# Performance work log

Hardware: AMD Instinct MI355X
Metric: run time of the kernel (lower is better)

Reference implementation:

```python
import jax, jax.numpy as jnp
import numpy as np

N, C, H, W = 4, 128, 64, 64
HEADS, KS, RED = 4, 7, 18
D = C // HEADS


def _layernorm(x, w, b, eps=1e-5):
    mu = x.mean(axis=-1, keepdims=True)
    var = ((x - mu) ** 2).mean(axis=-1, keepdims=True)
    return (x - mu) * jax.lax.rsqrt(var + eps) * w + b


def _gelu(x):
    return jax.nn.gelu(x, approximate=False)


def setup_inputs() -> dict:
    key = jax.random.key(0)
    ks = jax.random.split(key, 16)
    s = 0.02
    inp = {
        'x': jax.random.normal(ks[0], (N, C, H, W), jnp.float32),
        'ln1_w': jnp.ones((C,), jnp.float32), 'ln1_b': jnp.zeros((C,), jnp.float32),
        'ln2_w': jnp.ones((C,), jnp.float32), 'ln2_b': jnp.zeros((C,), jnp.float32),
        'qkv_w': jax.random.normal(ks[1], (C, 3 * C), jnp.float32) * s,
        'qkv_b': jnp.zeros((3 * C,), jnp.float32),
        'proj_w': jax.random.normal(ks[2], (C, C), jnp.float32) * s,
        'proj_b': jnp.zeros((C,), jnp.float32),
        'rpb': jax.random.normal(ks[3], (HEADS, 2 * KS - 1, 2 * KS - 1), jnp.float32) * s,
        'conv1_w': jax.random.normal(ks[4], (C, C // 4), jnp.float32) * s,
        'conv1_b': jnp.zeros((C // 4,), jnp.float32),
        'conv2_w': jax.random.normal(ks[5], (C // 4, C), jnp.float32) * s,
        'conv2_b': jnp.zeros((C,), jnp.float32),
        'ca1_w': jax.random.normal(ks[6], (C, C // RED), jnp.float32) * s,
        'ca1_b': jnp.zeros((C // RED,), jnp.float32),
        'ca2_w': jax.random.normal(ks[7], (C // RED, C), jnp.float32) * s,
        'ca2_b': jnp.zeros((C,), jnp.float32),
        'fc1_w': jax.random.normal(ks[8], (C, 4 * C), jnp.float32) * s,
        'fc1_b': jnp.zeros((4 * C,), jnp.float32),
        'fc2_w': jax.random.normal(ks[9], (4 * C, C), jnp.float32) * s,
        'fc2_b': jnp.zeros((C,), jnp.float32),
    }
    return inp


def _na2d(xc, qkv_w, qkv_b, rpb, proj_w, proj_b):
    # xc: [N, H, W, C] -> neighborhood attention with clamped k x k windows (NATTEN semantics)
    n, h, w, c = xc.shape
    qkv = (xc @ qkv_w + qkv_b).reshape(n, h, w, 3, HEADS, D)
    q, k, v = qkv[..., 0, :, :], qkv[..., 1, :, :], qkv[..., 2, :, :]
    q = q * (D ** -0.5)
    half = KS // 2
    ni = jnp.clip(jnp.arange(h) - half, 0, h - KS)          # window start per query row
    nj = jnp.clip(jnp.arange(w) - half, 0, w - KS)
    idx_i = ni[:, None] + jnp.arange(KS)                     # [H, KS]
    idx_j = nj[:, None] + jnp.arange(KS)                     # [W, KS]
    # gather key/value windows: [N, H, KS, W, KS, heads, D]
    kw = k[:, idx_i][:, :, :, idx_j]
    vw = v[:, idx_i][:, :, :, idx_j]
    attn = jnp.einsum('nijhd,niajbhd->nijhab', q, kw)        # [N,H,W,heads,KS,KS]
    bi = idx_i - jnp.arange(h)[:, None] + (KS - 1)           # rel-pos bias row index [H,KS]
    bj = idx_j - jnp.arange(w)[:, None] + (KS - 1)           # [W,KS]
    bias = rpb[:, bi][:, :, :, bj]                           # [heads,H,KS,W,KS]
    attn = attn + bias.transpose(1, 3, 0, 2, 4)[None]        # -> [1,H,W,heads,KS,KS]
    attn = jax.nn.softmax(attn.reshape(n, h, w, HEADS, KS * KS), axis=-1)
    attn = attn.reshape(n, h, w, HEADS, KS, KS)
    out = jnp.einsum('nijhab,niajbhd->nijhd', attn, vw).reshape(n, h, w, c)
    return out @ proj_w + proj_b


def reference(x, ln1_w, ln1_b, ln2_w, ln2_b, qkv_w, qkv_b, proj_w, proj_b, rpb,
              conv1_w, conv1_b, conv2_w, conv2_b, ca1_w, ca1_b, ca2_w, ca2_b,
              fc1_w, fc1_b, fc2_w, fc2_b):
    n, c, h, w = x.shape
    xs = x.transpose(0, 2, 3, 1).reshape(n, h * w, c)        # n (h w) c
    shortcut = xs
    xn = _layernorm(xs, ln1_w, ln1_b)
    xc = xn.reshape(n, h, w, c)
    # conv branch: 1x1 -> GELU -> 1x1 -> channel attention
    t = _gelu(xc @ conv1_w + conv1_b) @ conv2_w + conv2_b
    g = t.mean(axis=(1, 2))                                  # global avg pool [N,C]
    g = jax.nn.sigmoid(jax.nn.relu(g @ ca1_w + ca1_b) @ ca2_w + ca2_b)
    ca_x = (t * g[:, None, None, :]).reshape(n, h * w, c)
    # neighborhood attention branch
    na_x = _na2d(xc, qkv_w, qkv_b, rpb, proj_w, proj_b).reshape(n, h * w, c)
    x2 = shortcut + na_x + ca_x * 0.02
    m = _gelu(_layernorm(x2, ln2_w, ln2_b) @ fc1_w + fc1_b) @ fc2_w + fc2_b
    x3 = x2 + m
    return x3.reshape(n, h, w, c).transpose(0, 3, 1, 2)
```

## Files before the change

kernel.cpp:

```cpp
#include <hip/hip_runtime.h>
#include <hip/hip_bf16.h>
#include <math.h>

#define NB 4
#define CC 128
#define HH 64
#define WW 64
#define HEADS 4
#define KS 7
#define DD 32
#define HW 4096
#define MTOT 16384

typedef unsigned short BF;
typedef short short8 __attribute__((ext_vector_type(8)));
typedef float floatx4 __attribute__((ext_vector_type(4)));

__device__ __forceinline__ float gelu_f(float x) {
    return 0.5f * x * (1.0f + erff(x * 0.70710678118654752440f));
}

__device__ __forceinline__ BF f2bf(float f) {
    union { float f; unsigned u; } a; a.f = f;
    unsigned u = a.u;
    unsigned r = u + 0x7FFFu + ((u >> 16) & 1u);
    return (BF)(r >> 16);
}

__device__ __forceinline__ float bf2f(BF v) {
    return __uint_as_float(((unsigned)v) << 16);
}

#define LDK 40
#define LDK128 136

__global__ __launch_bounds__(256) void ln1t_kernel(
    const float* __restrict__ x, const float* __restrict__ w,
    const float* __restrict__ b, BF* __restrict__ out,
    float* __restrict__ part,
    const float* __restrict__ qkv_w, const float* __restrict__ conv1_w,
    const float* __restrict__ conv2_w, const float* __restrict__ proj_w,
    const float* __restrict__ fc1_w, const float* __restrict__ fc2_w,
    BF* __restrict__ qkvT, BF* __restrict__ c1T, BF* __restrict__ c2T,
    BF* __restrict__ projT2, BF* __restrict__ fc1T2, BF* __restrict__ fc2T2)
{
    const int blk = blockIdx.x;
    const int t  = threadIdx.x;

    if (blk >= 512) {
        for (int idx = (blk - 512) * 256 + t; idx < 204800; idx += 32768) {
            if (idx < 49152) {
                int l = idx, n = l >> 7, k = l & 127;
                qkvT[l] = f2bf(qkv_w[k * 384 + n]);
            } else if (idx < 53248) {
                int l = idx - 49152, n = l >> 7, k = l & 127;
                c1T[l] = f2bf(conv1_w[k * 32 + n]);
            } else if (idx < 57344) {
                int l = idx - 53248, n = l >> 5, k = l & 31;
                c2T[l] = f2bf(conv2_w[k * 128 + n]);
            } else if (idx < 73728) {
                int l = idx - 57344, kk = l & 31, n = (l >> 5) & 127, ks = l >> 12;
                projT2[l] = f2bf(proj_w[(ks * 32 + kk) * 128 + n]);
            } else if (idx < 139264) {
                int l = idx - 73728, kk = l & 31, n = (l >> 5) & 511, ks = l >> 14;
                fc1T2[l] = f2bf(fc1_w[(ks * 32 + kk) * 512 + n]);
            } else {
                int l = idx - 139264, kk = l & 31, n = (l >> 5) & 127, ks = l >> 12;
                fc2T2[l] = f2bf(fc2_w[(ks * 32 + kk) * 128 + n]);
            }
        }
        return;
    }

    __shared__ float xt[128][33];
    __shared__ float mus[32], rss[32];
    const int n  = blk >> 7;
    const int p0 = (blk & 127) * 32;
    if (blk < 4 && t < 128) part[blk * CC + t] = 0.f;

    {
        int pp = t & 31, c8 = t >> 5;
        #pragma unroll 4
        for (int it = 0; it < 16; it++) {
            int c = it * 8 + c8;
            xt[c][pp] = x[(size_t)(n * CC + c) * HW + p0 + pp];
        }
    }
    __syncthreads();
    {
        int pp2 = t >> 3, cb = t & 7;
        float s = 0.f;
        #pragma unroll
        for (int u = 0; u < 16; u++) s += xt[cb + u * 8][pp2];
        s += __shfl_xor(s, 1); s += __shfl_xor(s, 2); s += __shfl_xor(s, 4);
        float mu = s * (1.0f / CC);
        float v = 0.f;
        #pragma unroll
        for (int u = 0; u < 16; u++) { float d = xt[cb + u * 8][pp2] - mu; v += d * d; }
        v += __shfl_xor(v, 1); v += __shfl_xor(v, 2); v += __shfl_xor(v, 4);
        if (cb == 0) { mus[pp2] = mu; rss[pp2] = rsqrtf(v * (1.0f / CC) + 1e-5f); }
    }
    __syncthreads();
    {
        #pragma unroll
        for (int it = 0; it < 2; it++) {
            int pp2 = (t >> 4) + it * 16;
            int c0  = (t & 15) * 8;
            float mu = mus[pp2], rs = rss[pp2];
            int m = n * HW + p0 + pp2;
            short8 o;
            #pragma unroll
            for (int u = 0; u < 8; u++)
                o[u] = (short)f2bf((xt[c0 + u][pp2] - mu) * rs * w[c0 + u] + b[c0 + u]);
            *(short8*)(out + (size_t)m * CC + c0) = o;
        }
    }
}

template<int ACT>
__device__ __forceinline__ void k128_body(
    const BF* __restrict__ A, const BF* __restrict__ Bt,
    const float* __restrict__ bias, BF* __restrict__ Cout,
    int N, int row0, int col0, BF* Bl )
{
    const int t = threadIdx.x;
    const int w = t >> 6, lane = t & 63, q = lane >> 4, r16 = lane & 15;
    {
        int nn = t >> 2;
        int kk = (t & 3) * 32;
        const BF* src = Bt + (size_t)(col0 + nn) * 128 + kk;
        #pragma unroll
        for (int u = 0; u < 4; u++)
            *(uint4*)(Bl + nn * LDK128 + kk + u * 8) = *(const uint4*)(src + u * 8);
    }
    __syncthreads();
    floatx4 acc[4] = {};
    const BF* arow = A + (size_t)(row0 + w * 16 + r16) * CC;
    #pragma unroll
    for (int ks = 0; ks < 4; ks++) {
        short8 af = *(const short8*)(arow + ks * 32 + q * 8);
        #pragma unroll
        for (int nt = 0; nt < 4; nt++) {
            short8 bf = *(const short8*)(Bl + (nt * 16 + r16) * LDK128 + ks * 32 + q * 8);
            acc[nt] = __builtin_amdgcn_mfma_f32_16x16x32_bf16(af, bf, acc[nt], 0, 0, 0);
        }
    }
    #pragma unroll
    for (int nt = 0; nt < 4; nt++) {
        int col = col0 + nt * 16 + r16;
        float bv = bias[col];
        #pragma unroll
        for (int reg = 0; reg < 4; reg++) {
            int row = row0 + w * 16 + q * 4 + reg;
            float v = acc[nt][reg] + bv;
            if (ACT == 1) v = gelu_f(v);
            Cout[(size_t)row * N + col] = f2bf(v);
        }
    }
}

__global__ __launch_bounds__(256) void phase2(
    const BF* __restrict__ xn, const BF* __restrict__ qkvT,
    const float* __restrict__ qkv_b, BF* __restrict__ qkv_out,
    const BF* __restrict__ c1T, const float* __restrict__ b1,
    const BF* __restrict__ c2T, const float* __restrict__ b2,
    BF* __restrict__ tout, float* __restrict__ part)
{
    __shared__ __align__(16) char smem[26624];
    const int bid = blockIdx.x;
    const int t = threadIdx.x;
    const int w = t >> 6, lane = t & 63, q = lane >> 4, r16 = lane & 15;

    if (bid < 1536) {
        int col0 = (bid % 6) * 64;
        int row0 = (bid / 6) * 64;
        k128_body<0>(xn, qkvT, qkv_b, qkv_out, 384, row0, col0, (BF*)smem);
        return;
    }
    BF*    W1l = (BF*)smem;
    BF*    W2l = (BF*)(smem + 8704);
    BF*    Hl  = (BF*)(smem + 18944);
    float* red = (float*)(smem + 24064);
    const int row0 = (bid - 1536) * 64;
    {
        #pragma unroll
        for (int it = 0; it < 2; it++) {
            int idx = it * 256 + t;
            int nn = idx >> 4, u = idx & 15;
            *(uint4*)(W1l + nn * LDK128 + u * 8) = *(const uint4*)(c1T + nn * 128 + u * 8);
        }
    }
    {
        #pragma unroll
        for (int it = 0; it < 2; it++) {
            int idx = it * 256 + t;
            int nn = idx >> 2, u = idx & 3;
            *(uint4*)(W2l + nn * LDK + u * 8) = *(const uint4*)(c2T + nn * 32 + u * 8);
        }
    }
    __syncthreads();
    floatx4 a1[2] = {};
    const BF* arow = xn + (size_t)(row0 + w * 16 + r16) * CC;
    #pragma unroll
    for (int ks = 0; ks < 4; ks++) {
        short8 af = *(const short8*)(arow + ks * 32 + q * 8);
        #pragma unroll
        for (int nt = 0; nt < 2; nt++) {
            short8 bf = *(const short8*)(W1l + (nt * 16 + r16) * LDK128 + ks * 32 + q * 8);
            a1[nt] = __builtin_amdgcn_mfma_f32_16x16x32_bf16(af, bf, a1[nt], 0, 0, 0);
        }
    }
    #pragma unroll
    for (int nt = 0; nt < 2; nt++) {
        int col = nt * 16 + r16;
        float bv = b1[col];
        #pragma unroll
        for (int reg = 0; reg < 4; reg++)
            Hl[(w * 16 + q * 4 + reg) * LDK + col] = f2bf(gelu_f(a1[nt][reg] + bv));
    }
    __syncthreads();
    floatx4 a2[8] = {};
    short8 af2 = *(const short8*)(Hl + (w * 16 + r16) * LDK + q * 8);
    #pragma unroll
    for (int nt = 0; nt < 8; nt++) {
        short8 bf = *(const short8*)(W2l + (nt * 16 + r16) * LDK + q * 8);
        a2[nt] = __builtin_amdgcn_mfma_f32_16x16x32_bf16(af2, bf, a2[nt], 0, 0, 0);
    }
    #pragma unroll
    for (int nt = 0; nt < 8; nt++) {
        int col = nt * 16 + r16;
        float bv = b2[col];
        float s = 0.f;
        #pragma unroll
        for (int reg = 0; reg < 4; reg++) {
            int row = row0 + w * 16 + q * 4 + reg;
            float v = a2[nt][reg] + bv;
            tout[(size_t)row * CC + col] = f2bf(v);
            s += v;
        }
        s += __shfl_xor(s, 16);
        s += __shfl_xor(s, 32);
        if (lane < 16) red[w * 128 + col] = s;
    }
    __syncthreads();
    if (t < 128) {
        float cs = red[t] + red[128 + t] + red[256 + t] + red[384 + t];
        atomicAdd(&part[(row0 >> 12) * CC + t], cs);
    }
}

__global__ __launch_bounds__(256) void na_mfma_kernel(
    const BF* __restrict__ qkv, const float* __restrict__ rpb,
    BF* __restrict__ outp)
{
    __shared__ __align__(16) BF Kt[224][40];
    __shared__ __align__(16) BF Vt[32][232];
    __shared__ __align__(16) BF Qb[64][40];
    __shared__ __align__(16) BF Pl[4][16][232];
    __shared__ float rb[169];

    const int b = blockIdx.x;
    const int h = b & 3;
    const int tile = b >> 2;
    const int n = tile >> 6;
    const int ti = (tile >> 3) & 7, tj = tile & 7;
    const int t = threadIdx.x;
    const int w = t >> 6, lane = t & 63, quad = lane >> 4, r16 = lane & 15;
    const int i0 = ti * 8, j0 = tj * 8;
    const int wi0 = max(i0 - 3, 0), wj0 = max(j0 - 3, 0);
    const int R  = min(wi0 + 13, 63) - wi0 + 1;
    const int Rj = min(wj0 + 13, 63) - wj0 + 1;

    for (int idx = t; idx < 896; idx += 256) {
        int key = idx >> 2, ch = idx & 3;
        int kr = key >> 4, kc = key & 15;
        uint4 v = {0u, 0u, 0u, 0u};
        if (kr < R && kc < Rj) {
            size_t pix = (size_t)((n * HH + wi0 + kr) * WW + wj0 + kc);
            v = *(const uint4*)(qkv + pix * 384 + 128 + h * DD + ch * 8);
        }
        *(uint4*)&Kt[key][ch * 8] = v;
    }
    for (int idx = t; idx < 896; idx += 256) {
        int key = idx >> 2, ch = idx & 3;
        int kr = key >> 4, kc = key & 15;
        if (kr < R && kc < Rj) {
            size_t pix = (size_t)((n * HH + wi0 + kr) * WW + wj0 + kc);
            uint4 v = *(const uint4*)(qkv + pix * 384 + 256 + h * DD + ch * 8);
            const BF* pv = (const BF*)&v;
            #pragma unroll
            for (int u = 0; u < 8; u++) Vt[ch * 8 + u][key] = pv[u];
        } else {
            #pragma unroll
            for (int u = 0; u < 8; u++) Vt[ch * 8 + u][key] = 0;
        }
    }
    {
        int q = t >> 2, ch = t & 3;
        size_t mq = (size_t)((n * HH + i0 + (q >> 3)) * WW + j0 + (q & 7));
        *(uint4*)&Qb[q][ch * 8] = *(const uint4*)(qkv + mq * 384 + h * DD + ch * 8);
    }
    if (t < 169) rb[t] = rpb[h * 169 + t];
    __syncthreads();

    int oi[4], cok[4], bj0[4], ai_[4];
    #pragma unroll
    for (int reg = 0; reg < 4; reg++) {
        int q = w * 16 + quad * 4 + reg;
        int i = i0 + (q >> 3), j = j0 + (q & 7);
        int ni = min(max(i - 3, 0), HH - KS), nj = min(max(j - 3, 0), WW - KS);
        oi[reg]  = ni - wi0;
        ai_[reg] = ni - i + 6;
        int dc = r16 - (nj - wj0);
        cok[reg] = ((unsigned)dc < 7u) ? 1 : 0;
        bj0[reg] = min(max(dc + (nj - j + 6), 0), 12);
    }

    short8 aq = *(const short8*)&Qb[w * 16 + r16][quad * 8];
    floatx4 S[14];
    #pragma unroll
    for (int nt = 0; nt < 14; nt++) {
        floatx4 z = {0.f, 0.f, 0.f, 0.f};
        short8 bk = *(const short8*)&Kt[nt * 16 + r16][quad * 8];
        S[nt] = __builtin_amdgcn_mfma_f32_16x16x32_bf16(aq, bk, z, 0, 0, 0);
    }
    const float scale = 0.17677669529663688110f;
    #pragma unroll
    for (int nt = 0; nt < 14; nt++) {
        #pragma unroll
        for (int reg = 0; reg < 4; reg++) {
            int dr = nt - oi[reg];
            bool ok = ((unsigned)dr < 7u) && cok[reg];
            int bi = min(max(dr + ai_[reg], 0), 12);
            float bias = rb[bi * 13 + bj0[reg]];
            S[nt][reg] = ok ? fmaf(S[nt][reg], scale, bias) : -1e30f;
        }
    }
    float rinv[4];
    #pragma unroll
    for (int reg = 0; reg < 4; reg++) {
        float m = S[0][reg];
        #pragma unroll
        for (int nt = 1; nt < 14; nt++) m = fmaxf(m, S[nt][reg]);
        m = fmaxf(m, __shfl_xor(m, 1));
        m = fmaxf(m, __shfl_xor(m, 2));
        m = fmaxf(m, __shfl_xor(m, 4));
        m = fmaxf(m, __shfl_xor(m, 8));
        float s = 0.f;
        #pragma unroll
        for (int nt = 0; nt < 14; nt++) {
            float e = __expf(S[nt][reg] - m);
            S[nt][reg] = e;
            s += e;
        }
        s += __shfl_xor(s, 1);
        s += __shfl_xor(s, 2);
        s += __shfl_xor(s, 4);
        s += __shfl_xor(s, 8);
        rinv[reg] = 1.0f / s;
    }
    #pragma unroll
    for (int nt = 0; nt < 14; nt++)
        #pragma unroll
        for (int reg = 0; reg < 4; reg++)
            Pl[w][quad * 4 + reg][nt * 16 + r16] = f2bf(S[nt][reg] * rinv[reg]);

    floatx4 O0 = {0.f, 0.f, 0.f, 0.f}, O1 = {0.f, 0.f, 0.f, 0.f};
    #pragma unroll
    for (int ks = 0; ks < 7; ks++) {
        short8 ap = *(const short8*)&Pl[w][r16][ks * 32 + quad * 8];
        short8 b0 = *(const short8*)&Vt[r16][ks * 32 + quad * 8];
        short8 b1 = *(const short8*)&Vt[16 + r16][ks * 32 + quad * 8];
        O0 = __builtin_amdgcn_mfma_f32_16x16x32_bf16(ap, b0, O0, 0, 0, 0);
        O1 = __builtin_amdgcn_mfma_f32_16x16x32_bf16(ap, b1, O1, 0, 0, 0);
    }
    #pragma unroll
    for (int reg = 0; reg < 4; reg++) {
        int q = w * 16 + quad * 4 + reg;
        size_t m = (size_t)((n * HH + i0 + (q >> 3)) * WW + j0 + (q & 7));
        outp[m * CC + h * DD + r16]      = f2bf(O0[reg]);
        outp[m * CC + h * DD + 16 + r16] = f2bf(O1[reg]);
    }
}

__global__ __launch_bounds__(256) void tail_kernel(
    const BF* __restrict__ A, const BF* __restrict__ projT2,
    const float* __restrict__ proj_b, const float* __restrict__ x,
    const BF* __restrict__ tbuf, const float* __restrict__ part,
    const float* __restrict__ ca1_w, const float* __restrict__ ca1_b,
    const float* __restrict__ ca2_w, const float* __restrict__ ca2_b,
    const float* __restrict__ w2, const float* __restrict__ b2,
    const BF* __restrict__ fc1T2, const float* __restrict__ fc1_b,
    const BF* __restrict__ fc2T2, const float* __restrict__ fc2_b,
    float* __restrict__ out)
{
    __shared__ float xs[32][132];
    __shared__ __align__(16) BF ln2l[32][136];
    __shared__ __align__(16) BF hl[32][520];
    __shared__ float st[128][34];
    __shared__ float gs[128], h1s[7], gl[128];
    __shared__ float S1[4][16], S2[4][16];

    const int t = threadIdx.x;
    const int w = t >> 6, lane = t & 63, quad = lane >> 4, r16 = lane & 15;
    const int row0 = blockIdx.x * 32;
    const int n = row0 >> 12, p0 = row0 & 4095;
    const int mt = w & 1, nh = w >> 1;
    const int lr0 = mt * 16;

    #pragma unroll
    for (int it = 0; it < 4; it++) {
        int idx4 = it * 256 + t;
        int p4 = idx4 & 7, c = idx4 >> 3;
        float4 v = *(const float4*)(x + (size_t)(n * CC + c) * HW + p0 + p4 * 4);
        xs[p4 * 4 + 0][c] = v.x; xs[p4 * 4 + 1][c] = v.y;
        xs[p4 * 4 + 2][c] = v.z; xs[p4 * 4 + 3][c] = v.w;
    }
    if (t < 128) gs[t] = part[n * CC + t] * (1.0f / HW);
    __syncthreads();
    if (t < 7) {
        float a = ca1_b[t];
        for (int k = 0; k < 128; k++) a += gs[k] * ca1_w[k * 7 + t];
        h1s[t] = fmaxf(a, 0.f);
    }
    __syncthreads();
    if (t < 128) {
        float o = ca2_b[t];
        #pragma unroll
        for (int r = 0; r < 7; r++) o += h1s[r] * ca2_w[r * 128 + t];
        gl[t] = 1.0f / (1.0f + expf(-o));
    }

    floatx4 acc[4] = {};
    const BF* arow = A + (size_t)(row0 + lr0 + r16) * CC;
    #pragma unroll
    for (int ks = 0; ks < 4; ks++) {
        short8 af = *(const short8*)(arow + ks * 32 + quad * 8);
        #pragma unroll
        for (int nt = 0; nt < 4; nt++) {
            int col = nh * 64 + nt * 16 + r16;
            short8 bf = *(const short8*)(projT2 + ((size_t)(ks * 128 + col)) * 32 + quad * 8);
            acc[nt] = __builtin_amdgcn_mfma_f32_16x16x32_bf16(af, bf, acc[nt], 0, 0, 0);
        }
    }
    __syncthreads();

    float x2r[4][4];
    float s1[4] = {0.f, 0.f, 0.f, 0.f}, s2[4] = {0.f, 0.f, 0.f, 0.f};
    #pragma unroll
    for (int nt = 0; nt < 4; nt++) {
        int col = nh * 64 + nt * 16 + r16;
        float bv = proj_b[col], gv = gl[col];
        #pragma unroll
        for (int reg = 0; reg < 4; reg++) {
            int lr = lr0 + quad * 4 + reg;
            float tv = bf2f(tbuf[(size_t)(row0 + lr) * CC + col]);
            float v = acc[nt][reg] + bv + xs[lr][col] + 0.02f * tv * gv;
            x2r[nt][reg] = v;
            s1[reg] += v; s2[reg] += v * v;
        }
    }
    #pragma unroll
    for (int reg = 0; reg < 4; reg++) {
        #pragma unroll
        for (int off = 8; off; off >>= 1) {
            s1[reg] += __shfl_xor(s1[reg], off);
            s2[reg] += __shfl_xor(s2[reg], off);
        }
    }
    if (r16 == 0) {
        #pragma unroll
        for (int reg = 0; reg < 4; reg++) {
            S1[w][quad * 4 + reg] = s1[reg];
            S2[w][quad * 4 + reg] = s2[reg];
        }
    }
    __syncthreads();
    const int pw = w ^ 2;
    float mu[4], rr[4];
    #pragma unroll
    for (int reg = 0; reg < 4; reg++) {
        int r = quad * 4 + reg;
        float t1 = S1[w][r] + S1[pw][r];
        float t2 = S2[w][r] + S2[pw][r];
        mu[reg] = t1 * (1.0f / CC);
        float var = t2 * (1.0f / CC) - mu[reg] * mu[reg];
        rr[reg] = rsqrtf(var + 1e-5f);
    }
    #pragma unroll
    for (int nt = 0; nt < 4; nt++) {
        int col = nh * 64 + nt * 16 + r16;
        float wv = w2[col], bv2 = b2[col];
        #pragma unroll
        for (int reg = 0; reg < 4; reg++) {
            int lr = lr0 + quad * 4 + reg;
            ln2l[lr][col] = f2bf((x2r[nt][reg] - mu[reg]) * rr[reg] * wv + bv2);
        }
    }
    __syncthreads();

    short8 af1[4];
    #pragma unroll
    for (int ks = 0; ks < 4; ks++)
        af1[ks] = *(const short8*)&ln2l[lr0 + r16][ks * 32 + quad * 8];
    #pragma unroll
    for (int g = 0; g < 4; g++) {
        floatx4 a2[4] = {};
        #pragma unroll
        for (int ks = 0; ks < 4; ks++) {
            #pragma unroll
            for (int nt = 0; nt < 4; nt++) {
                int col = nh * 256 + g * 64 + nt * 16 + r16;
                short8 bf = *(const short8*)(fc1T2 + ((size_t)(ks * 512 + col)) * 32 + quad * 8);
                a2[nt] = __builtin_amdgcn_mfma_f32_16x16x32_bf16(af1[ks], bf, a2[nt], 0, 0, 0);
            }
        }
        #pragma unroll
        for (int nt = 0; nt < 4; nt++) {
            int col = nh * 256 + g * 64 + nt * 16 + r16;
            float bv = fc1_b[col];
            #pragma unroll
            for (int reg = 0; reg < 4; reg++) {
                int lr = lr0 + quad * 4 + reg;
                hl[lr][col] = f2bf(gelu_f(a2[nt][reg] + bv));
            }
        }
    }
    __syncthreads();

    floatx4 a3[4] = {};
    #pragma unroll
    for (int ks = 0; ks < 16; ks++) {
        short8 af = *(const short8*)&hl[lr0 + r16][ks * 32 + quad * 8];
        #pragma unroll
        for (int nt = 0; nt < 4; nt++) {
            int col = nh * 64 + nt * 16 + r16;
            short8 bf = *(const short8*)(fc2T2 + ((size_t)(ks * 128 + col)) * 32 + quad * 8);
            a3[nt] = __builtin_amdgcn_mfma_f32_16x16x32_bf16(af, bf, a3[nt], 0, 0, 0);
        }
    }
    #pragma unroll
    for (int nt = 0; nt < 4; nt++) {
        int col = nh * 64 + nt * 16 + r16;
        float bv = fc2_b[col];
        #pragma unroll
        for (int reg = 0; reg < 4; reg++) {
            int lr = lr0 + quad * 4 + reg;
            st[col][lr] = a3[nt][reg] + bv + x2r[nt][reg];
        }
    }
    __syncthreads();
    {
        int col = t >> 1, ch = (t & 1) * 16;
        float* dst = out + (size_t)(n * CC + col) * HW + p0 + ch;
        #pragma unroll
        for (int u = 0; u < 4; u++) {
            float4 v;
            v.x = st[col][ch + u * 4 + 0];
            v.y = st[col][ch + u * 4 + 1];
            v.z = st[col][ch + u * 4 + 2];
            v.w = st[col][ch + u * 4 + 3];
            *(float4*)(dst + u * 4) = v;
        }
    }
}

extern "C" void kernel_launch(void* const* d_in, const int* in_sizes, int n_in,
                              void* d_out, int out_size, void* d_ws, size_t ws_size,
                              hipStream_t stream)
{
    const float* x       = (const float*)d_in[0];
    const float* ln1_w   = (const float*)d_in[1];
    const float* ln1_b   = (const float*)d_in[2];
    const float* ln2_w   = (const float*)d_in[3];
    const float* ln2_b   = (const float*)d_in[4];
    const float* qkv_w   = (const float*)d_in[5];
    const float* qkv_b   = (const float*)d_in[6];
    const float* proj_w  = (const float*)d_in[7];
    const float* proj_b  = (const float*)d_in[8];
    const float* rpb     = (const float*)d_in[9];
    const float* conv1_w = (const float*)d_in[10];
    const float* conv1_b = (const float*)d_in[11];
    const float* conv2_w = (const float*)d_in[12];
    const float* conv2_b = (const float*)d_in[13];
    const float* ca1_w   = (const float*)d_in[14];
    const float* ca1_b   = (const float*)d_in[15];
    const float* ca2_w   = (const float*)d_in[16];
    const float* ca2_b   = (const float*)d_in[17];
    const float* fc1_w   = (const float*)d_in[18];
    const float* fc1_b   = (const float*)d_in[19];
    const float* fc2_w   = (const float*)d_in[20];
    const float* fc2_b   = (const float*)d_in[21];
    float* out = (float*)d_out;

    char* ws = (char*)d_ws;
    BF*    xn_bf   = (BF*)(ws);
    BF*    qkv_bf  = (BF*)(ws + 4194304);
    BF*    t_bf    = (BF*)(ws + 16777216);
    BF*    na_bf   = (BF*)(ws + 20971520);
    float* part    = (float*)(ws + 25165824);
    BF*    qkvT    = (BF*)(ws + 25167872);
    BF*    c1T     = (BF*)(ws + 25266176);
    BF*    c2T     = (BF*)(ws + 25274368);
    BF*    projT2  = (BF*)(ws + 25282560);
    BF*    fc1T2   = (BF*)(ws + 25315328);
    BF*    fc2T2   = (BF*)(ws + 25446400);

    ln1t_kernel<<<640, 256, 0, stream>>>(x, ln1_w, ln1_b, xn_bf, part,
        qkv_w, conv1_w, conv2_w, proj_w, fc1_w, fc2_w,
        qkvT, c1T, c2T, projT2, fc1T2, fc2T2);
    phase2<<<1792, 256, 0, stream>>>(xn_bf, qkvT, qkv_b, qkv_bf,
                                     c1T, conv1_b, c2T, conv2_b, t_bf, part);
    na_mfma_kernel<<<1024, 256, 0, stream>>>(qkv_bf, rpb, na_bf);
    tail_kernel<<<512, 256, 0, stream>>>(na_bf, projT2, proj_b, x, t_bf, part,
                                         ca1_w, ca1_b, ca2_w, ca2_b,
                                         ln2_w, ln2_b, fc1T2, fc1_b,
                                         fc2T2, fc2_b, out);
}
```

Baseline: 172.6 us.

## Fuse four kernels into one cooperative persistent kernel with grid syncs

Replaces the four separate launches (LN1 plus weight transposes, QKV/conv GEMMs, neighborhood attention, tail MLP) with a single cooperative kernel of 512 blocks. Each phase is separated by grid.sync(), and blocks loop over the former grid sizes. The weight transposes are spread across all 512 blocks instead of a dedicated extra set. The aim is to remove inter-kernel launch gaps and tail effects. The cost is grid-wide barrier overhead, a reduced grid that may limit latency hiding, and 68KB of shared memory per block with a launch bound of 2 blocks per CU.

Result: slower. 387.7 us (+124.6%).

```diff
diff --git a/kernel.cpp b/kernel.cpp
--- a/kernel.cpp
+++ b/kernel.cpp
@@ -1,6 +1,9 @@
 #include <hip/hip_runtime.h>
 #include <hip/hip_bf16.h>
+#include <hip/hip_cooperative_groups.h>
 #include <math.h>
+
+namespace cg = cooperative_groups;
 
 #define NB 4
 #define CC 128
@@ -34,533 +37,515 @@
 #define LDK 40
 #define LDK128 136
 
-__global__ __launch_bounds__(256) void ln1t_kernel(
-    const float* __restrict__ x, const float* __restrict__ w,
-    const float* __restrict__ b, BF* __restrict__ out,
-    float* __restrict__ part,
-    const float* __restrict__ qkv_w, const float* __restrict__ conv1_w,
-    const float* __restrict__ conv2_w, const float* __restrict__ proj_w,
-    const float* __restrict__ fc1_w, const float* __restrict__ fc2_w,
-    BF* __restrict__ qkvT, BF* __restrict__ c1T, BF* __restrict__ c2T,
-    BF* __restrict__ projT2, BF* __restrict__ fc1T2, BF* __restrict__ fc2T2)
+struct Params {
+    const float* x;
+    const float* ln1_w; const float* ln1_b;
+    const float* ln2_w; const float* ln2_b;
+    const float* qkv_b; const float* proj_b;
+    const float* rpb;
+    const float* conv1_b; const float* conv2_b;
+    const float* ca1_w; const float* ca1_b;
+    const float* ca2_w; const float* ca2_b;
+    const float* fc1_b; const float* fc2_b;
+    const float* qkv_w; const float* conv1_w; const float* conv2_w;
+    const float* proj_w; const float* fc1_w; const float* fc2_w;
+    BF* xn; BF* qkv; BF* tbuf; BF* na;
+    float* part;
+    BF* qkvT; BF* c1T; BF* c2T; BF* projT2; BF* fc1T2; BF* fc2T2;
+    float* out;
+};
+
+#define SMEM_BYTES 68352
+
+__global__ __launch_bounds__(256, 2) void mega_kernel(Params p)
 {
+    __shared__ __align__(16) char smem[SMEM_BYTES];
     const int blk = blockIdx.x;
-    const int t  = threadIdx.x;
-
-    if (blk >= 512) {
-        for (int idx = (blk - 512) * 256 + t; idx < 204800; idx += 32768) {
+    const int t   = threadIdx.x;
+    const int w = t >> 6, lane = t & 63, quad = lane >> 4, r16 = lane & 15;
+    cg::grid_group grid = cg::this_grid();
+
+    {
+        float* xt  = (float*)smem;
+        float* mus = (float*)(smem + 16896);
+        float* rss = (float*)(smem + 17024);
+        const int n  = blk >> 7;
+        const int p0 = (blk & 127) * 32;
+        if (blk < 4 && t < 128) p.part[blk * CC + t] = 0.f;
+
+        {
+            int pp = t & 31, c8 = t >> 5;
+            #pragma unroll 4
+            for (int it = 0; it < 16; it++) {
+                int c = it * 8 + c8;
+                xt[c * 33 + pp] = p.x[(size_t)(n * CC + c) * HW + p0 + pp];
+            }
+        }
+        for (int idx = blk * 400 + t; idx < (blk + 1) * 400; idx += 256) {
             if (idx < 49152) {
-                int l = idx, n = l >> 7, k = l & 127;
-                qkvT[l] = f2bf(qkv_w[k * 384 + n]);
+                int l = idx, nn = l >> 7, k = l & 127;
+                p.qkvT[l] = f2bf(p.qkv_w[k * 384 + nn]);
             } else if (idx < 53248) {
-                int l = idx - 49152, n = l >> 7, k = l & 127;
-                c1T[l] = f2bf(conv1_w[k * 32 + n]);
+                int l = idx - 49152, nn = l >> 7, k = l & 127;
+                p.c1T[l] = f2bf(p.conv1_w[k * 32 + nn]);
             } else if (idx < 57344) {
-                int l = idx - 53248, n = l >> 5, k = l & 31;
-                c2T[l] = f2bf(conv2_w[k * 128 + n]);
+                int l = idx - 53248, nn = l >> 5, k = l & 31;
+                p.c2T[l] = f2bf(p.conv2_w[k * 128 + nn]);
             } else if (idx < 73728) {
-                int l = idx - 57344, kk = l & 31, n = (l >> 5) & 127, ks = l >> 12;
-                projT2[l] = f2bf(proj_w[(ks * 32 + kk) * 128 + n]);
+                int l = idx - 57344, kk = l & 31, nn = (l >> 5) & 127, ks = l >> 12;
+                p.projT2[l] = f2bf(p.proj_w[(ks * 32 + kk) * 128 + nn]);
             } else if (idx < 139264) {
-                int l = idx - 73728, kk = l & 31, n = (l >> 5) & 511, ks = l >> 14;
-                fc1T2[l] = f2bf(fc1_w[(ks * 32 + kk) * 512 + n]);
+                int l = idx - 73728, kk = l & 31, nn = (l >> 5) & 511, ks = l >> 14;
+                p.fc1T2[l] = f2bf(p.fc1_w[(ks * 32 + kk) * 512 + nn]);
+            } else if (idx < 204800) {
+                int l = idx - 139264, kk = l & 31, nn = (l >> 5) & 127, ks = l >> 12;
+                p.fc2T2[l] = f2bf(p.fc2_w[(ks * 32 + kk) * 128 + nn]);
+            }
+        }
+        __syncthreads();
+        {
+            int pp2 = t >> 3, cb = t & 7;
+            float s = 0.f;
+            #pragma unroll
+            for (int u = 0; u < 16; u++) s += xt[(cb + u * 8) * 33 + pp2];
+            s += __shfl_xor(s, 1); s += __shfl_xor(s, 2); s += __shfl_xor(s, 4);
+            float mu = s * (1.0f / CC);
+            float v = 0.f;
+            #pragma unroll
+            for (int u = 0; u < 16; u++) { float d = xt[(cb + u * 8) * 33 + pp2] - mu; v += d * d; }
+            v += __shfl_xor(v, 1); v += __shfl_xor(v, 2); v += __shfl_xor(v, 4);
+            if (cb == 0) { mus[pp2] = mu; rss[pp2] = rsqrtf(v * (1.0f / CC) + 1e-5f); }
+        }
+        __syncthreads();
+        {
+            #pragma unroll
+            for (int it = 0; it < 2; it++) {
+                int pp2 = (t >> 4) + it * 16;
+                int c0  = (t & 15) * 8;
+                float mu = mus[pp2], rs = rss[pp2];
+                int m = n * HW + p0 + pp2;
+                short8 o;
+                #pragma unroll
+                for (int u = 0; u < 8; u++)
+                    o[u] = (short)f2bf((xt[(c0 + u) * 33 + pp2] - mu) * rs * p.ln1_w[c0 + u] + p.ln1_b[c0 + u]);
+                *(short8*)(p.xn + (size_t)m * CC + c0) = o;
+            }
+        }
+    }
+    grid.sync();
+
+    for (int bid = blk; bid < 1792; bid += 512) {
+        if (bid < 1536) {
+            BF* Bl = (BF*)smem;
+            const int col0 = (bid % 6) * 64;
+            const int row0 = (bid / 6) * 64;
+            {
+                int nn = t >> 2, kk = (t & 3) * 32;
+                const BF* src = p.qkvT + (size_t)(col0 + nn) * 128 + kk;
+                #pragma unroll
+                for (int u = 0; u < 4; u++)
+                    *(uint4*)(Bl + nn * LDK128 + kk + u * 8) = *(const uint4*)(src + u * 8);
+            }
+            __syncthreads();
+            floatx4 acc[4] = {};
+            const BF* arow = p.xn + (size_t)(row0 + w * 16 + r16) * CC;
+            #pragma unroll
+            for (int ks = 0; ks < 4; ks++) {
+                short8 af = *(const short8*)(arow + ks * 32 + quad * 8);
+                #pragma unroll
+                for (int nt = 0; nt < 4; nt++) {
+                    short8 bf = *(const short8*)(Bl + (nt * 16 + r16) * LDK128 + ks * 32 + quad * 8);
+                    acc[nt] = __builtin_amdgcn_mfma_f32_16x16x32_bf16(af, bf, acc[nt], 0, 0, 0);
+                }
+            }
+            #pragma unroll
+            for (int nt = 0; nt < 4; nt++) {
+                int col = col0 + nt * 16 + r16;
+                float bv = p.qkv_b[col];
+                #pragma unroll
+                for (int reg = 0; reg < 4; reg++) {
+                    int row = row0 + w * 16 + quad * 4 + reg;
+                    p.qkv[(size_t)row * 384 + col] = f2bf(acc[nt][reg] + bv);
+                }
+            }
+            __syncthreads();
+        } else {
+            BF*    W1l = (BF*)smem;
+            BF*    W2l = (BF*)(smem + 8704);
+            BF*    Hl  = (BF*)(smem + 18944);
+            float* red = (float*)(smem + 24064);
+            const int row0 = (bid - 1536) * 64;
+            {
+                #pragma unroll
+                for (int it = 0; it < 2; it++) {
+                    int idx = it * 256 + t;
+                    int nn = idx >> 4, u = idx & 15;
+                    *(uint4*)(W1l + nn * LDK128 + u * 8) = *(const uint4*)(p.c1T + nn * 128 + u * 8);
+                }
+            }
+            {
+                #pragma unroll
+                for (int it = 0; it < 2; it++) {
+                    int idx = it * 256 + t;
+                    int nn = idx >> 2, u = idx & 3;
+                    *(uint4*)(W2l + nn * LDK + u * 8) = *(const uint4*)(p.c2T + nn * 32 + u * 8);
+                }
+            }
+            __syncthreads();
+            floatx4 a1[2] = {};
+            const BF* arow = p.xn + (size_t)(row0 + w * 16 + r16) * CC;
+            #pragma unroll
+            for (int ks = 0; ks < 4; ks++) {
+                short8 af = *(const short8*)(arow + ks * 32 + quad * 8);
+                #pragma unroll
+                for (int nt = 0; nt < 2; nt++) {
+                    short8 bf = *(const short8*)(W1l + (nt * 16 + r16) * LDK128 + ks * 32 + quad * 8);
+                    a1[nt] = __builtin_amdgcn_mfma_f32_16x16x32_bf16(af, bf, a1[nt], 0, 0, 0);
+                }
+            }
+            #pragma unroll
+            for (int nt = 0; nt < 2; nt++) {
+                int col = nt * 16 + r16;
+                float bv = p.conv1_b[col];
+                #pragma unroll
+                for (int reg = 0; reg < 4; reg++)
+                    Hl[(w * 16 + quad * 4 + reg) * LDK + col] = f2bf(gelu_f(a1[nt][reg] + bv));
+            }
+            __syncthreads();
+            floatx4 a2[8] = {};
+            short8 af2 = *(const short8*)(Hl + (w * 16 + r16) * LDK + quad * 8);
+            #pragma unroll
+            for (int nt = 0; nt < 8; nt++) {
+                short8 bf = *(const short8*)(W2l + (nt * 16 + r16) * LDK + quad * 8);
+                a2[nt] = __builtin_amdgcn_mfma_f32_16x16x32_bf16(af2, bf, a2[nt], 0, 0, 0);
+            }
+            #pragma unroll
+            for (int nt = 0; nt < 8; nt++) {
+                int col = nt * 16 + r16;
+                float bv = p.conv2_b[col];
+                float s = 0.f;
+                #pragma unroll
+                for (int reg = 0; reg < 4; reg++) {
+                    int row = row0 + w * 16 + quad * 4 + reg;
+                    float v = a2[nt][reg] + bv;
+                    p.tbuf[(size_t)row * CC + col] = f2bf(v);
+                    s += v;
+                }
+                s += __shfl_xor(s, 16);
+                s += __shfl_xor(s, 32);
+                if (lane < 16) red[w * 128 + col] = s;
+            }
+            __syncthreads();
+            if (t < 128) {
+                float cs = red[t] + red[128 + t] + red[256 + t] + red[384 + t];
+                atomicAdd(&p.part[(row0 >> 12) * CC + t], cs);
+            }
+            __syncthreads();
+        }
+    }
+    grid.sync();
+
+    for (int bid = blk; bid < 1024; bid += 512) {
+        BF*    Kt = (BF*)smem;
+        BF*    Vt = (BF*)(smem + 17920);
+        BF*    Qb = (BF*)(smem + 32768);
+        BF*    Pl = (BF*)(smem + 37888);
+        float* rb = (float*)(smem + 67584);
+
+        const int h = bid & 3;
+        const int tile = bid >> 2;
+        const int n = tile >> 6;
+        const int ti = (tile >> 3) & 7, tj = tile & 7;
+        const int i0 = ti * 8, j0 = tj * 8;
+        const int wi0 = max(i0 - 3, 0), wj0 = max(j0 - 3, 0);
+        const int R  = min(wi0 + 13, 63) - wi0 + 1;
+        const int Rj = min(wj0 + 13, 63) - wj0 + 1;
+
+        for (int idx = t; idx < 896; idx += 256) {
+            int key = idx >> 2, ch = idx & 3;
+            int kr = key >> 4, kc = key & 15;
+            uint4 v = {0u, 0u, 0u, 0u};
+            if (kr < R && kc < Rj) {
+                size_t pix = (size_t)((n * HH + wi0 + kr) * WW + wj0 + kc);
+                v = *(const uint4*)(p.qkv + pix * 384 + 128 + h * DD + ch * 8);
+            }
+            *(uint4*)(Kt + key * 40 + ch * 8) = v;
+        }
+        for (int idx = t; idx < 896; idx += 256) {
+            int key = idx >> 2, ch = idx & 3;
+            int kr = key >> 4, kc = key & 15;
+            if (kr < R && kc < Rj) {
+                size_t pix = (size_t)((n * HH + wi0 + kr) * WW + wj0 + kc);
+                uint4 v = *(const uint4*)(p.qkv + pix * 384 + 256 + h * DD + ch * 8);
+                const BF* pv = (const BF*)&v;
+                #pragma unroll
+                for (int u = 0; u < 8; u++) Vt[(ch * 8 + u) * 232 + key] = pv[u];
             } else {
-                int l = idx - 139264, kk = l & 31, n = (l >> 5) & 127, ks = l >> 12;
-                fc2T2[l] = f2bf(fc2_w[(ks * 32 + kk) * 128 + n]);
-            }
-        }
-        return;
+                #pragma unroll
+                for (int u = 0; u < 8; u++) Vt[(ch * 8 + u) * 232 + key] = 0;
+            }
+        }
+        {
+            int q = t >> 2, ch = t & 3;
+            size_t mq = (size_t)((n * HH + i0 + (q >> 3)) * WW + j0 + (q & 7));
+            *(uint4*)(Qb + q * 40 + ch * 8) = *(const uint4*)(p.qkv + mq * 384 + h * DD + ch * 8);
+        }
+        if (t < 169) rb[t] = p.rpb[h * 169 + t];
+        __syncthreads();
+
+        int oi[4], cok[4], bj0[4], ai_[4];
+        #pragma unroll
+        for (int reg = 0; reg < 4; reg++) {
+            int q = w * 16 + quad * 4 + reg;
+            int i = i0 + (q >> 3), j = j0 + (q & 7);
+            int ni = min(max(i - 3, 0), HH - KS), nj = min(max(j - 3, 0), WW - KS);
+            oi[reg]  = ni - wi0;
+            ai_[reg] = ni - i + 6;
+            int dc = r16 - (nj - wj0);
+            cok[reg] = ((unsigned)dc < 7u) ? 1 : 0;
+            bj0[reg] = min(max(dc + (nj - j + 6), 0), 12);
+        }
+
+        short8 aq = *(const short8*)(Qb + (w * 16 + r16) * 40 + quad * 8);
+        floatx4 S[14];
+        #pragma unroll
+        for (int nt = 0; nt < 14; nt++) {
+            floatx4 z = {0.f, 0.f, 0.f, 0.f};
+            short8 bk = *(const short8*)(Kt + (nt * 16 + r16) * 40 + quad * 8);
+            S[nt] = __builtin_amdgcn_mfma_f32_16x16x32_bf16(aq, bk, z, 0, 0, 0);
+        }
+        const float scale = 0.17677669529663688110f;
+        #pragma unroll
+        for (int nt = 0; nt < 14; nt++) {
+            #pragma unroll
+            for (int reg = 0; reg < 4; reg++) {
+                int dr = nt - oi[reg];
+                bool ok = ((unsigned)dr < 7u) && cok[reg];
+                int bi = min(max(dr + ai_[reg], 0), 12);
+                float bias = rb[bi * 13 + bj0[reg]];
+                S[nt][reg] = ok ? fmaf(S[nt][reg], scale, bias) : -1e30f;
+            }
+        }
+        float rinv[4];
+        #pragma unroll
+        for (int reg = 0; reg < 4; reg++) {
+            float m = S[0][reg];
+            #pragma unroll
+            for (int nt = 1; nt < 14; nt++) m = fmaxf(m, S[nt][reg]);
+            m = fmaxf(m, __shfl_xor(m, 1));
+            m = fmaxf(m, __shfl_xor(m, 2));
+            m = fmaxf(m, __shfl_xor(m, 4));
+            m = fmaxf(m, __shfl_xor(m, 8));
+            float s = 0.f;
+            #pragma unroll
+            for (int nt = 0; nt < 14; nt++) {
+                float e = __expf(S[nt][reg] - m);
+                S[nt][reg] = e;
+                s += e;
+            }
+            s += __shfl_xor(s, 1);
+            s += __shfl_xor(s, 2);
+            s += __shfl_xor(s, 4);
+            s += __shfl_xor(s, 8);
+            rinv[reg] = 1.0f / s;
+        }
+        #pragma unroll
+        for (int nt = 0; nt < 14; nt++)
+            #pragma unroll
+            for (int reg = 0; reg < 4; reg++)
+                Pl[(w * 16 + quad * 4 + reg) * 232 + nt * 16 + r16] = f2bf(S[nt][reg] * rinv[reg]);
+
+        floatx4 O0 = {0.f, 0.f, 0.f, 0.f}, O1 = {0.f, 0.f, 0.f, 0.f};
+        #pragma unroll
+        for (int ks = 0; ks < 7; ks++) {
+            short8 ap = *(const short8*)(Pl + (w * 16 + r16) * 232 + ks * 32 + quad * 8);
+            short8 b0 = *(const short8*)(Vt + r16 * 232 + ks * 32 + quad * 8);
+            short8 b1 = *(const short8*)(Vt + (16 + r16) * 232 + ks * 32 + quad * 8);
+            O0 = __builtin_amdgcn_mfma_f32_16x16x32_bf16(ap, b0, O0, 0, 0, 0);
+            O1 = __builtin_amdgcn_mfma_f32_16x16x32_bf16(ap, b1, O1, 0, 0, 0);
+        }
+        #pragma unroll
+        for (int reg = 0; reg < 4; reg++) {
+            int q = w * 16 + quad * 4 + reg;
+            size_t m = (size_t)((n * HH + i0 + (q >> 3)) * WW + j0 + (q & 7));
+            p.na[m * CC + h * DD + r16]      = f2bf(O0[reg]);
+            p.na[m * CC + h * DD + 16 + r16] = f2bf(O1[reg]);
+        }
+        __syncthreads();
     }
-
-    __shared__ float xt[128][33];
-    __shared__ float mus[32], rss[32];
-    const int n  = blk >> 7;
-    const int p0 = (blk & 127) * 32;
-    if (blk < 4 && t < 128) part[blk * CC + t] = 0.f;
+    grid.sync();
 
     {
-        int pp = t & 31, c8 = t >> 5;
-        #pragma unroll 4
-        for (int it = 0; it < 16; it++) {
-            int c = it * 8 + c8;
-            xt[c][pp] = x[(size_t)(n * CC + c) * HW + p0 + pp];
-        }
-    }
-    __syncthreads();
-    {
-        int pp2 = t >> 3, cb = t & 7;
-        float s = 0.f;
-        #pragma unroll
-        for (int u = 0; u < 16; u++) s += xt[cb + u * 8][pp2];
-        s += __shfl_xor(s, 1); s += __shfl_xor(s, 2); s += __shfl_xor(s, 4);
-        float mu = s * (1.0f / CC);
-        float v = 0.f;
-        #pragma unroll
-        for (int u = 0; u < 16; u++) { float d = xt[cb + u * 8][pp2] - mu; v += d * d; }
-        v += __shfl_xor(v, 1); v += __shfl_xor(v, 2); v += __shfl_xor(v, 4);
-        if (cb == 0) { mus[pp2] = mu; rss[pp2] = rsqrtf(v * (1.0f / CC) + 1e-5f); }
-    }
-    __syncthreads();
-    {
-        #pragma unroll
-        for (int it = 0; it < 2; it++) {
-            int pp2 = (t >> 4) + it * 16;
-            int c0  = (t & 15) * 8;
-            float mu = mus[pp2], rs = rss[pp2];
-            int m = n * HW + p0 + pp2;
-            short8 o;
-            #pragma unroll
-            for (int u = 0; u < 8; u++)
-                o[u] = (short)f2bf((xt[c0 + u][pp2] - mu) * rs * w[c0 + u] + b[c0 + u]);
-            *(short8*)(out + (size_t)m * CC + c0) = o;
-        }
-    }
-}
-
-template<int ACT>
-__device__ __forceinline__ void k128_body(
-    const BF* __restrict__ A, const BF* __restrict__ Bt,
-    const float* __restrict__ bias, BF* __restrict__ Cout,
-    int N, int row0, int col0, BF* Bl )
-{
-    const int t = threadIdx.x;
-    const int w = t >> 6, lane = t & 63, q = lane >> 4, r16 = lane & 15;
-    {
-        int nn = t >> 2;
-        int kk = (t & 3) * 32;
-        const BF* src = Bt + (size_t)(col0 + nn) * 128 + kk;
-        #pragma unroll
-        for (int u = 0; u < 4; u++)
-            *(uint4*)(Bl + nn * LDK128 + kk + u * 8) = *(const uint4*)(src + u * 8);
-    }
-    __syncthreads();
-    floatx4 acc[4] = {};
-    const BF* arow = A + (size_t)(row0 + w * 16 + r16) * CC;
-    #pragma unroll
-    for (int ks = 0; ks < 4; ks++) {
-        short8 af = *(const short8*)(arow + ks * 32 + q * 8);
-        #pragma unroll
-        for (int nt = 0; nt < 4; nt++) {
-            short8 bf = *(const short8*)(Bl + (nt * 16 + r16) * LDK128 + ks * 32 + q * 8);
-            acc[nt] = __builtin_amdgcn_mfma_f32_16x16x32_bf16(af, bf, acc[nt], 0, 0, 0);
-        }
-    }
-    #pragma unroll
-    for (int nt = 0; nt < 4; nt++) {
-        int col = col0 + nt * 16 + r16;
-        float bv = bias[col];
-        #pragma unroll
-        for (int reg = 0; reg < 4; reg++) {
-            int row = row0 + w * 16 + q * 4 + reg;
-            float v = acc[nt][reg] + bv;
-            if (ACT == 1) v = gelu_f(v);
-            Cout[(size_t)row * N + col] = f2bf(v);
-        }
-    }
-}
-
-__global__ __launch_bounds__(256) void phase2(
-    const BF* __restrict__ xn, const BF* __restrict__ qkvT,
-    const float* __restrict__ qkv_b, BF* __restrict__ qkv_out,
-    const BF* __restrict__ c1T, const float* __restrict__ b1,
-    const BF* __restrict__ c2T, const float* __restrict__ b2,
-    BF* __restrict__ tout, float* __restrict__ part)
-{
-    __shared__ __align__(16) char smem[26624];
-    const int bid = blockIdx.x;
-    const int t = threadIdx.x;
-    const int w = t >> 6, lane = t & 63, q = lane >> 4, r16 = lane & 15;
-
-    if (bid < 1536) {
-        int col0 = (bid % 6) * 64;
-        int row0 = (bid / 6) * 64;
-        k128_body<0>(xn, qkvT, qkv_b, qkv_out, 384, row0, col0, (BF*)smem);
-        return;
-    }
-    BF*    W1l = (BF*)smem;
-    BF*    W2l = (BF*)(smem + 8704);
-    BF*    Hl  = (BF*)(smem + 18944);
-    float* red = (float*)(smem + 24064);
-    const int row0 = (bid - 1536) * 64;
-    {
-        #pragma unroll
-        for (int it = 0; it < 2; it++) {
-            int idx = it * 256 + t;
-            int nn = idx >> 4, u = idx & 15;
-            *(uint4*)(W1l + nn * LDK128 + u * 8) = *(const uint4*)(c1T + nn * 128 + u * 8);
-        }
-    }
-    {
-        #pragma unroll
-        for (int it = 0; it < 2; it++) {
-            int idx = it * 256 + t;
-            int nn = idx >> 2, u = idx & 3;
-            *(uint4*)(W2l + nn * LDK + u * 8) = *(const uint4*)(c2T + nn * 32 + u * 8);
-        }
-    }
-    __syncthreads();
-    floatx4 a1[2] = {};
-    const BF* arow = xn + (size_t)(row0 + w * 16 + r16) * CC;
-    #pragma unroll
-    for (int ks = 0; ks < 4; ks++) {
-        short8 af = *(const short8*)(arow + ks * 32 + q * 8);
-        #pragma unroll
-        for (int nt = 0; nt < 2; nt++) {
-            short8 bf = *(const short8*)(W1l + (nt * 16 + r16) * LDK128 + ks * 32 + q * 8);
-            a1[nt] = __builtin_amdgcn_mfma_f32_16x16x32_bf16(af, bf, a1[nt], 0, 0, 0);
-        }
-    }
-    #pragma unroll
-    for (int nt = 0; nt < 2; nt++) {
-        int col = nt * 16 + r16;
-        float bv = b1[col];
-        #pragma unroll
-        for (int reg = 0; reg < 4; reg++)
-            Hl[(w * 16 + q * 4 + reg) * LDK + col] = f2bf(gelu_f(a1[nt][reg] + bv));
-    }
-    __syncthreads();
-    floatx4 a2[8] = {};
-    short8 af2 = *(const short8*)(Hl + (w * 16 + r16) * LDK + q * 8);
-    #pragma unroll
-    for (int nt = 0; nt < 8; nt++) {
-        short8 bf = *(const short8*)(W2l + (nt * 16 + r16) * LDK + q * 8);
-        a2[nt] = __builtin_amdgcn_mfma_f32_16x16x32_bf16(af2, bf, a2[nt], 0, 0, 0);
-    }
-    #pragma unroll
-    for (int nt = 0; nt < 8; nt++) {
-        int col = nt * 16 + r16;
-        float bv = b2[col];
-        float s = 0.f;
-        #pragma unroll
-        for (int reg = 0; reg < 4; reg++) {
-            int row = row0 + w * 16 + q * 4 + reg;
-            float v = a2[nt][reg] + bv;
-            tout[(size_t)row * CC + col] = f2bf(v);
-            s += v;
-        }
-        s += __shfl_xor(s, 16);
-        s += __shfl_xor(s, 32);
-        if (lane < 16) red[w * 128 + col] = s;
-    }
-    __syncthreads();
-    if (t < 128) {
-        float cs = red[t] + red[128 + t] + red[256 + t] + red[384 + t];
-        atomicAdd(&part[(row0 >> 12) * CC + t], cs);
-    }
-}
-
-__global__ __launch_bounds__(256) void na_mfma_kernel(
-    const BF* __restrict__ qkv, const float* __restrict__ rpb,
-    BF* __restrict__ outp)
-{
-    __shared__ __align__(16) BF Kt[224][40];
-    __shared__ __align__(16) BF Vt[32][232];
-    __shared__ __align__(16) BF Qb[64][40];
-    __shared__ __align__(16) BF Pl[4][16][232];
-    __shared__ float rb[169];
-
-    const int b = blockIdx.x;
-    const int h = b & 3;
-    const int tile = b >> 2;
-    const int n = tile >> 6;
-    const int ti = (tile >> 3) & 7, tj = tile & 7;
-    const int t = threadIdx.x;
-    const int w = t >> 6, lane = t & 63, quad = lane >> 4, r16 = lane & 15;
-    const int i0 = ti * 8, j0 = tj * 8;
-    const int wi0 = max(i0 - 3, 0), wj0 = max(j0 - 3, 0);
-    const int R  = min(wi0 + 13, 63) - wi0 + 1;
-    const int Rj = min(wj0 + 13, 63) - wj0 + 1;
-
-    for (int idx = t; idx < 896; idx += 256) {
-        int key = idx >> 2, ch = idx & 3;
-        int kr = key >> 4, kc = key & 15;
-        uint4 v = {0u, 0u, 0u, 0u};
-        if (kr < R && kc < Rj) {
-            size_t pix = (size_t)((n * HH + wi0 + kr) * WW + wj0 + kc);
-            v = *(const uint4*)(qkv + pix * 384 + 128 + h * DD + ch * 8);
-        }
-        *(uint4*)&Kt[key][ch * 8] = v;
-    }
-    for (int idx = t; idx < 896; idx += 256) {
-        int key = idx >> 2, ch = idx & 3;
-        int kr = key >> 4, kc = key & 15;
-        if (kr < R && kc < Rj) {
-            size_t pix = (size_t)((n * HH + wi0 + kr) * WW + wj0 + kc);
-            uint4 v = *(const uint4*)(qkv + pix * 384 + 256 + h * DD + ch * 8);
-            const BF* pv = (const BF*)&v;
-            #pragma unroll
-            for (int u = 0; u < 8; u++) Vt[ch * 8 + u][key] = pv[u];
-        } else {
-            #pragma unroll
-            for (int u = 0; u < 8; u++) Vt[ch * 8 + u][key] = 0;
-        }
-    }
-    {
-        int q = t >> 2, ch = t & 3;
-        size_t mq = (size_t)((n * HH + i0 + (q >> 3)) * WW + j0 + (q & 7));
-        *(uint4*)&Qb[q][ch * 8] = *(const uint4*)(qkv + mq * 384 + h * DD + ch * 8);
-    }
-    if (t < 169) rb[t] = rpb[h * 169 + t];
-    __syncthreads();
-
-    int oi[4], cok[4], bj0[4], ai_[4];
-    #pragma unroll
-    for (int reg = 0; reg < 4; reg++) {
-        int q = w * 16 + quad * 4 + reg;
-        int i = i0 + (q >> 3), j = j0 + (q & 7);
-        int ni = min(max(i - 3, 0), HH - KS), nj = min(max(j - 3, 0), WW - KS);
-        oi[reg]  = ni - wi0;
-        ai_[reg] = ni - i + 6;
-        int dc = r16 - (nj - wj0);
-        cok[reg] = ((unsigned)dc < 7u) ? 1 : 0;
-        bj0[reg] = min(max(dc + (nj - j + 6), 0), 12);
-    }
-
-    short8 aq = *(const short8*)&Qb[w * 16 + r16][quad * 8];
-    floatx4 S[14];
-    #pragma unroll
-    for (int nt = 0; nt < 14; nt++) {
-        floatx4 z = {0.f, 0.f, 0.f, 0.f};
-        short8 bk = *(const short8*)&Kt[nt * 16 + r16][quad * 8];
-        S[nt] = __builtin_amdgcn_mfma_f32_16x16x32_bf16(aq, bk, z, 0, 0, 0);
-    }
-    const float scale = 0.17677669529663688110f;
-    #pragma unroll
-    for (int nt = 0; nt < 14; nt++) {
-        #pragma unroll
-        for (int reg = 0; reg < 4; reg++) {
-            int dr = nt - oi[reg];
-            bool ok = ((unsigned)dr < 7u) && cok[reg];
-            int bi = min(max(dr + ai_[reg], 0), 12);
-            float bias = rb[bi * 13 + bj0[reg]];
-            S[nt][reg] = ok ? fmaf(S[nt][reg], scale, bias) : -1e30f;
-        }
-    }
-    float rinv[4];
-    #pragma unroll
-    for (int reg = 0; reg < 4; reg++) {
-        float m = S[0][reg];
-        #pragma unroll
-        for (int nt = 1; nt < 14; nt++) m = fmaxf(m, S[nt][reg]);
-        m = fmaxf(m, __shfl_xor(m, 1));
-        m = fmaxf(m, __shfl_xor(m, 2));
-        m = fmaxf(m, __shfl_xor(m, 4));
-        m = fmaxf(m, __shfl_xor(m, 8));
-        float s = 0.f;
-        #pragma unroll
-        for (int nt = 0; nt < 14; nt++) {
-            float e = __expf(S[nt][reg] - m);
-            S[nt][reg] = e;
-            s += e;
-        }
-        s += __shfl_xor(s, 1);
-        s += __shfl_xor(s, 2);
-        s += __shfl_xor(s, 4);
-        s += __shfl_xor(s, 8);
-        rinv[reg] = 1.0f / s;
-    }
-    #pragma unroll
-    for (int nt = 0; nt < 14; nt++)
-        #pragma unroll
-        for (int reg = 0; reg < 4; reg++)
-            Pl[w][quad * 4 + reg][nt * 16 + r16] = f2bf(S[nt][reg] * rinv[reg]);
-
-    floatx4 O0 = {0.f, 0.f, 0.f, 0.f}, O1 = {0.f, 0.f, 0.f, 0.f};
-    #pragma unroll
-    for (int ks = 0; ks < 7; ks++) {
-        short8 ap = *(const short8*)&Pl[w][r16][ks * 32 + quad * 8];
-        short8 b0 = *(const short8*)&Vt[r16][ks * 32 + quad * 8];
-        short8 b1 = *(const short8*)&Vt[16 + r16][ks * 32 + quad * 8];
-        O0 = __builtin_amdgcn_mfma_f32_16x16x32_bf16(ap, b0, O0, 0, 0, 0);
-        O1 = __builtin_amdgcn_mfma_f32_16x16x32_bf16(ap, b1, O1, 0, 0, 0);
-    }
-    #pragma unroll
-    for (int reg = 0; reg < 4; reg++) {
-        int q = w * 16 + quad * 4 + reg;
-        size_t m = (size_t)((n * HH + i0 + (q >> 3)) * WW + j0 + (q & 7));
-        outp[m * CC + h * DD + r16]      = f2bf(O0[reg]);
-        outp[m * CC + h * DD + 16 + r16] = f2bf(O1[reg]);
-    }
-}
-
-__global__ __launch_bounds__(256) void tail_kernel(
-    const BF* __restrict__ A, const BF* __restrict__ projT2,
-    const float* __restrict__ proj_b, const float* __restrict__ x,
-    const BF* __restrict__ tbuf, const float* __restrict__ part,
-    const float* __restrict__ ca1_w, const float* __restrict__ ca1_b,
-    const float* __restrict__ ca2_w, const float* __restrict__ ca2_b,
-    const float* __restrict__ w2, const float* __restrict__ b2,
-    const BF* __restrict__ fc1T2, const float* __restrict__ fc1_b,
-    const BF* __restrict__ fc2T2, const float* __restrict__ fc2_b,
-    float* __restrict__ out)
-{
-    __shared__ float xs[32][132];
-    __shared__ __align__(16) BF ln2l[32][136];
-    __shared__ __align__(16) BF hl[32][520];
-    __shared__ float st[128][34];
-    __shared__ float gs[128], h1s[7], gl[128];
-    __shared__ float S1[4][16], S2[4][16];
-
-    const int t = threadIdx.x;
-    const int w = t >> 6, lane = t & 63, quad = lane >> 4, r16 = lane & 15;
-    const int row0 = blockIdx.x * 32;
-    const int n = row0 >> 12, p0 = row0 & 4095;
-    const int mt = w & 1, nh = w >> 1;
-    const int lr0 = mt * 16;
-
-    #pragma unroll
-    for (int it = 0; it < 4; it++) {
-        int idx4 = it * 256 + t;
-        int p4 = idx4 & 7, c = idx4 >> 3;
-        float4 v = *(const float4*)(x + (size_t)(n * CC + c) * HW + p0 + p4 * 4);
-        xs[p4 * 4 + 0][c] = v.x; xs[p4 * 4 + 1][c] = v.y;
-        xs[p4 * 4 + 2][c] = v.z; xs[p4 * 4 + 3][c] = v.w;
-    }
-    if (t < 128) gs[t] = part[n * CC + t] * (1.0f / HW);
-    __syncthreads();
-    if (t < 7) {
-        float a = ca1_b[t];
-        for (int k = 0; k < 128; k++) a += gs[k] * ca1_w[k * 7 + t];
-        h1s[t] = fmaxf(a, 0.f);
-    }
-    __syncthreads();
-    if (t < 128) {
-        float o = ca2_b[t];
-        #pragma unroll
-        for (int r = 0; r < 7; r++) o += h1s[r] * ca2_w[r * 128 + t];
-        gl[t] = 1.0f / (1.0f + expf(-o));
-    }
-
-    floatx4 acc[4] = {};
-    const BF* arow = A + (size_t)(row0 + lr0 + r16) * CC;
-    #pragma unroll
-    for (int ks = 0; ks < 4; ks++) {
-        short8 af = *(const short8*)(arow + ks * 32 + quad * 8);
+        float* xs   = (float*)smem;
+        float* st   = (float*)smem;
+        BF*    ln2l = (BF*)(smem + 17408);
+        BF*    hl   = (BF*)(smem + 26112);
+        float* gs   = (float*)(smem + 59392);
+        float* h1s  = (float*)(smem + 59904);
+        float* gl   = (float*)(smem + 59936);
+        float* S1   = (float*)(smem + 60448);
+        float* S2   = (float*)(smem + 60704);
+
+        const int row0 = blk * 32;
+        const int n = row0 >> 12, p0 = row0 & 4095;
+        const int mt = w & 1, nh = w >> 1;
+        const int lr0 = mt * 16;
+
+        #pragma unroll
+        for (int it = 0; it < 4; it++) {
+            int idx4 = it * 256 + t;
+            int p4 = idx4 & 7, c = idx4 >> 3;
+            float4 v = *(const float4*)(p.x + (size_t)(n * CC + c) * HW + p0 + p4 * 4);
+            xs[(p4 * 4 + 0) * 132 + c] = v.x; xs[(p4 * 4 + 1) * 132 + c] = v.y;
+            xs[(p4 * 4 + 2) * 132 + c] = v.z; xs[(p4 * 4 + 3) * 132 + c] = v.w;
+        }
+        if (t < 128) gs[t] = p.part[n * CC + t] * (1.0f / HW);
+        __syncthreads();
+        if (t < 7) {
+            float a = p.ca1_b[t];
+            for (int k = 0; k < 128; k++) a += gs[k] * p.ca1_w[k * 7 + t];
+            h1s[t] = fmaxf(a, 0.f);
+        }
+        __syncthreads();
+        if (t < 128) {
+            float o = p.ca2_b[t];
+            #pragma unroll
+            for (int r = 0; r < 7; r++) o += h1s[r] * p.ca2_w[r * 128 + t];
+            gl[t] = 1.0f / (1.0f + expf(-o));
+        }
+
+        floatx4 acc[4] = {};
+        const BF* arow = p.na + (size_t)(row0 + lr0 + r16) * CC;
+        #pragma unroll
+        for (int ks = 0; ks < 4; ks++) {
+            short8 af = *(const short8*)(arow + ks * 32 + quad * 8);
+            #pragma unroll
+            for (int nt = 0; nt < 4; nt++) {
+                int col = nh * 64 + nt * 16 + r16;
+                short8 bf = *(const short8*)(p.projT2 + ((size_t)(ks * 128 + col)) * 32 + quad * 8);
+                acc[nt] = __builtin_amdgcn_mfma_f32_16x16x32_bf16(af, bf, acc[nt], 0, 0, 0);
+            }
+        }
+        __syncthreads();
+
+        float x2r[4][4];
+        float s1[4] = {0.f, 0.f, 0.f, 0.f}, s2[4] = {0.f, 0.f, 0.f, 0.f};
         #pragma unroll
         for (int nt = 0; nt < 4; nt++) {
             int col = nh * 64 + nt * 16 + r16;
-            short8 bf = *(const short8*)(projT2 + ((size_t)(ks * 128 + col)) * 32 + quad * 8);
-            acc[nt] = __builtin_amdgcn_mfma_f32_16x16x32_bf16(af, bf, acc[nt], 0, 0, 0);
-        }
-    }
-    __syncthreads();
-
-    float x2r[4][4];
-    float s1[4] = {0.f, 0.f, 0.f, 0.f}, s2[4] = {0.f, 0.f, 0.f, 0.f};
-    #pragma unroll
-    for (int nt = 0; nt < 4; nt++) {
-        int col = nh * 64 + nt * 16 + r16;
-        float bv = proj_b[col], gv = gl[col];
+            float bv = p.proj_b[col], gv = gl[col];
+            #pragma unroll
+            for (int reg = 0; reg < 4; reg++) {
+                int lr = lr0 + quad * 4 + reg;
+                float tv = bf2f(p.tbuf[(size_t)(row0 + lr) * CC + col]);
+                float v = acc[nt][reg] + bv + xs[lr * 132 + col] + 0.02f * tv * gv;
+                x2r[nt][reg] = v;
+                s1[reg] += v; s2[reg] += v * v;
+            }
+        }
         #pragma unroll
         for (int reg = 0; reg < 4; reg++) {
-            int lr = lr0 + quad * 4 + reg;
-            float tv = bf2f(tbuf[(size_t)(row0 + lr) * CC + col]);
-            float v = acc[nt][reg] + bv + xs[lr][col] + 0.02f * tv * gv;
-            x2r[nt][reg] = v;
-            s1[reg] += v; s2[reg] += v * v;
-        }
-    }
-    #pragma unroll
-    for (int reg = 0; reg < 4; reg++) {
-        #pragma unroll
-        for (int off = 8; off; off >>= 1) {
-            s1[reg] += __shfl_xor(s1[reg], off);
-            s2[reg] += __shfl_xor(s2[reg], off);
-        }
-    }
-    if (r16 == 0) {
+            #pragma unroll
+            for (int off = 8; off; off >>= 1) {
+                s1[reg] += __shfl_xor(s1[reg], off);
+                s2[reg] += __shfl_xor(s2[reg], off);
+            }
+        }
+        if (r16 == 0) {
+            #pragma unroll
+            for (int reg = 0; reg < 4; reg++) {
+                S1[w * 16 + quad * 4 + reg] = s1[reg];
+                S2[w * 16 + quad * 4 + reg] = s2[reg];
+            }
+        }
+        __syncthreads();
+        const int pw = w ^ 2;
+        float mu[4], rr[4];
         #pragma unroll
         for (int reg = 0; reg < 4; reg++) {
-            S1[w][quad * 4 + reg] = s1[reg];
-            S2[w][quad * 4 + reg] = s2[reg];
-        }
-    }
-    __syncthreads();
-    const int pw = w ^ 2;
-    float mu[4], rr[4];
-    #pragma unroll
-    for (int reg = 0; reg < 4; reg++) {
-        int r = quad * 4 + reg;
-        float t1 = S1[w][r] + S1[pw][r];
-        float t2 = S2[w][r] + S2[pw][r];
-        mu[reg] = t1 * (1.0f / CC);
-        float var = t2 * (1.0f / CC) - mu[reg] * mu[reg];
-        rr[reg] = rsqrtf(var + 1e-5f);
-    }
-    #pragma unroll
-    for (int nt = 0; nt < 4; nt++) {
-        int col = nh * 64 + nt * 16 + r16;
-        float wv = w2[col], bv2 = b2[col];
-        #pragma unroll
-        for (int reg = 0; reg < 4; reg++) {
-            int lr = lr0 + quad * 4 + reg;
-            ln2l[lr][col] = f2bf((x2r[nt][reg] - mu[reg]) * rr[reg] * wv + bv2);
-        }
-    }
-    __syncthreads();
-
-    short8 af1[4];
-    #pragma unroll
-    for (int ks = 0; ks < 4; ks++)
-        af1[ks] = *(const short8*)&ln2l[lr0 + r16][ks * 32 + quad * 8];
-    #pragma unroll
-    for (int g = 0; g < 4; g++) {
-        floatx4 a2[4] = {};
-        #pragma unroll
-        for (int ks = 0; ks < 4; ks++) {
+            int r = quad * 4 + reg;
+            float t1 = S1[w * 16 + r] + S1[pw * 16 + r];
+            float t2 = S2[w * 16 + r] + S2[pw * 16 + r];
+            mu[reg] = t1 * (1.0f / CC);
+            float var = t2 * (1.0f / CC) - mu[reg] * mu[reg];
+            rr[reg] = rsqrtf(var + 1e-5f);
+        }
+        #pragma unroll
+        for (int nt = 0; nt < 4; nt++) {
+            int col = nh * 64 + nt * 16 + r16;
+            float wv = p.ln2_w[col], bv2 = p.ln2_b[col];
+            #pragma unroll
+            for (int reg = 0; reg < 4; reg++) {
+                int lr = lr0 + quad * 4 + reg;
+                ln2l[lr * 136 + col] = f2bf((x2r[nt][reg] - mu[reg]) * rr[reg] * wv + bv2);
+            }
+        }
+        __syncthreads();
+
+        short8 af1[4];
+        #pragma unroll
+        for (int ks = 0; ks < 4; ks++)
+            af1[ks] = *(const short8*)(ln2l + (lr0 + r16) * 136 + ks * 32 + quad * 8);
+        #pragma unroll
+        for (int g = 0; g < 4; g++) {
+            floatx4 a2[4] = {};
+            #pragma unroll
+            for (int ks = 0; ks < 4; ks++) {
+                #pragma unroll
+                for (int nt = 0; nt < 4; nt++) {
+                    int col = nh * 256 + g * 64 + nt * 16 + r16;
+                    short8 bf = *(const short8*)(p.fc1T2 + ((size_t)(ks * 512 + col)) * 32 + quad * 8);
+                    a2[nt] = __builtin_amdgcn_mfma_f32_16x16x32_bf16(af1[ks], bf, a2[nt], 0, 0, 0);
+                }
+            }
             #pragma unroll
             for (int nt = 0; nt < 4; nt++) {
                 int col = nh * 256 + g * 64 + nt * 16 + r16;
-                short8 bf = *(const short8*)(fc1T2 + ((size_t)(ks * 512 + col)) * 32 + quad * 8);
-                a2[nt] = __builtin_amdgcn_mfma_f32_16x16x32_bf16(af1[ks], bf, a2[nt], 0, 0, 0);
-            }
-        }
+                float bv = p.fc1_b[col];
+                #pragma unroll
+                for (int reg = 0; reg < 4; reg++) {
+                    int lr = lr0 + quad * 4 + reg;
+                    hl[lr * 520 + col] = f2bf(gelu_f(a2[nt][reg] + bv));
+                }
+            }
+        }
+        __syncthreads();
+
+        floatx4 a3[4] = {};
+        #pragma unroll
+        for (int ks = 0; ks < 16; ks++) {
+            short8 af = *(const short8*)(hl + (lr0 + r16) * 520 + ks * 32 + quad * 8);
+            #pragma unroll
+            for (int nt = 0; nt < 4; nt++) {
+                int col = nh * 64 + nt * 16 + r16;
+                short8 bf = *(const short8*)(p.fc2T2 + ((size_t)(ks * 128 + col)) * 32 + quad * 8);
+                a3[nt] = __builtin_amdgcn_mfma_f32_16x16x32_bf16(af, bf, a3[nt], 0, 0, 0);
+            }
+        }
+        __syncthreads();
         #pragma unroll
         for (int nt = 0; nt < 4; nt++) {
-            int col = nh * 256 + g * 64 + nt * 16 + r16;
-            float bv = fc1_b[col];
+            int col = nh * 64 + nt * 16 + r16;
+            float bv = p.fc2_b[col];
             #pragma unroll
             for (int reg = 0; reg < 4; reg++) {
                 int lr = lr0 + quad * 4 + reg;
-                hl[lr][col] = f2bf(gelu_f(a2[nt][reg] + bv));
-            }
-        }
-    }
-    __syncthreads();
-
-    floatx4 a3[4] = {};
-    #pragma unroll
-    for (int ks = 0; ks < 16; ks++) {
-        short8 af = *(const short8*)&hl[lr0 + r16][ks * 32 + quad * 8];
-        #pragma unroll
-        for (int nt = 0; nt < 4; nt++) {
-            int col = nh * 64 + nt * 16 + r16;
-            short8 bf = *(const short8*)(fc2T2 + ((size_t)(ks * 128 + col)) * 32 + quad * 8);
-            a3[nt] = __builtin_amdgcn_mfma_f32_16x16x32_bf16(af, bf, a3[nt], 0, 0, 0);
-        }
-    }
-    #pragma unroll
-    for (int nt = 0; nt < 4; nt++) {
-        int col = nh * 64 + nt * 16 + r16;
-        float bv = fc2_b[col];
-        #pragma unroll
-        for (int reg = 0; reg < 4; reg++) {
-            int lr = lr0 + quad * 4 + reg;
-            st[col][lr] = a3[nt][reg] + bv + x2r[nt][reg];
-        }
-    }
-    __syncthreads();
-    {
-        int col = t >> 1, ch = (t & 1) * 16;
-        float* dst = out + (size_t)(n * CC + col) * HW + p0 + ch;
-        #pragma unroll
-        for (int u = 0; u < 4; u++) {
-            float4 v;
-            v.x = st[col][ch + u * 4 + 0];
-            v.y = st[col][ch + u * 4 + 1];
-            v.z = st[col][ch + u * 4 + 2];
-            v.w = st[col][ch + u * 4 + 3];
-            *(float4*)(dst + u * 4) = v;
+                st[col * 34 + lr] = a3[nt][reg] + bv + x2r[nt][reg];
+            }
+        }
+        __syncthreads();
+        {
+            int col = t >> 1, ch = (t & 1) * 16;
+            float* dst = p.out + (size_t)(n * CC + col) * HW + p0 + ch;
+            #pragma unroll
+            for (int u = 0; u < 4; u++) {
+                float4 v;
+                v.x = st[col * 34 + ch + u * 4 + 0];
+                v.y = st[col * 34 + ch + u * 4 + 1];
+                v.z = st[col * 34 + ch + u * 4 + 2];
+                v.w = st[col * 34 + ch + u * 4 + 3];
+                *(float4*)(dst + u * 4) = v;
+            }
         }
     }
 }
@@ -569,51 +554,45 @@
                               void* d_out, int out_size, void* d_ws, size_t ws_size,
                               hipStream_t stream)
 {
-    const float* x       = (const float*)d_in[0];
-    const float* ln1_w   = (const float*)d_in[1];
-    const float* ln1_b   = (const float*)d_in[2];
-    const float* ln2_w   = (const float*)d_in[3];
-    const float* ln2_b   = (const float*)d_in[4];
-    const float* qkv_w   = (const float*)d_in[5];
-    const float* qkv_b   = (const float*)d_in[6];
-    const float* proj_w  = (const float*)d_in[7];
-    const float* proj_b  = (const float*)d_in[8];
-    const float* rpb     = (const float*)d_in[9];
-    const float* conv1_w = (const float*)d_in[10];
-    const float* conv1_b = (const float*)d_in[11];
-    const float* conv2_w = (const float*)d_in[12];
-    const float* conv2_b = (const float*)d_in[13];
-    const float* ca1_w   = (const float*)d_in[14];
-    const float* ca1_b   = (const float*)d_in[15];
-    const float* ca2_w   = (const float*)d_in[16];
-    const float* ca2_b   = (const float*)d_in[17];
-    const float* fc1_w   = (const float*)d_in[18];
-    const float* fc1_b   = (const float*)d_in[19];
-    const float* fc2_w   = (const float*)d_in[20];
-    const float* fc2_b   = (const float*)d_in[21];
-    float* out = (float*)d_out;
-
     char* ws = (char*)d_ws;
-    BF*    xn_bf   = (BF*)(ws);
-    BF*    qkv_bf  = (BF*)(ws + 4194304);
-    BF*    t_bf    = (BF*)(ws + 16777216);
-    BF*    na_bf   = (BF*)(ws + 20971520);
-    float* part    = (float*)(ws + 25165824);
-    BF*    qkvT    = (BF*)(ws + 25167872);
-    BF*    c1T     = (BF*)(ws + 25266176);
-    BF*    c2T     = (BF*)(ws + 25274368);
-    BF*    projT2  = (BF*)(ws + 25282560);
-    BF*    fc1T2   = (BF*)(ws + 25315328);
-    BF*    fc2T2   = (BF*)(ws + 25446400);
-
-    ln1t_kernel<<<640, 256, 0, stream>>>(x, ln1_w, ln1_b, xn_bf, part,
-        qkv_w, conv1_w, conv2_w, proj_w, fc1_w, fc2_w,
-        qkvT, c1T, c2T, projT2, fc1T2, fc2T2);
-    phase2<<<1792, 256, 0, stream>>>(xn_bf, qkvT, qkv_b, qkv_bf,
-                                     c1T, conv1_b, c2T, conv2_b, t_bf, part);
-    na_mfma_kernel<<<1024, 256, 0, stream>>>(qkv_bf, rpb, na_bf);
-    tail_kernel<<<512, 256, 0, stream>>>(na_bf, projT2, proj_b, x, t_bf, part,
-                                         ca1_w, ca1_b, ca2_w, ca2_b,
-                                         ln2_w, ln2_b, fc1T2, fc1_b,
-                                         fc2T2, fc2_b, out);
+    Params p;
+    p.x       = (const float*)d_in[0];
+    p.ln1_w   = (const float*)d_in[1];
+    p.ln1_b   = (const float*)d_in[2];
+    p.ln2_w   = (const float*)d_in[3];
+    p.ln2_b   = (const float*)d_in[4];
+    p.qkv_w   = (const float*)d_in[5];
+    p.qkv_b   = (const float*)d_in[6];
+    p.proj_w  = (const float*)d_in[7];
+    p.proj_b  = (const float*)d_in[8];
+    p.rpb     = (const float*)d_in[9];
+    p.conv1_w = (const float*)d_in[10];
+    p.conv1_b = (const float*)d_in[11];
+    p.conv2_w = (const float*)d_in[12];
+    p.conv2_b = (const float*)d_in[13];
+    p.ca1_w   = (const float*)d_in[14];
+    p.ca1_b   = (const float*)d_in[15];
+    p.ca2_w   = (const float*)d_in[16];
+    p.ca2_b   = (const float*)d_in[17];
+    p.fc1_w   = (const float*)d_in[18];
+    p.fc1_b   = (const float*)d_in[19];
+    p.fc2_w   = (const float*)d_in[20];
+    p.fc2_b   = (const float*)d_in[21];
+    p.out     = (float*)d_out;
+
+    p.xn     = (BF*)(ws);
+    p.qkv    = (BF*)(ws + 4194304);
+    p.tbuf   = (BF*)(ws + 16777216);
+    p.na     = (BF*)(ws + 20971520);
+    p.part   = (float*)(ws + 25165824);
+    p.qkvT   = (BF*)(ws + 25167872);
+    p.c1T    = (BF*)(ws + 25266176);
+    p.c2T    = (BF*)(ws + 25274368);
+    p.projT2 = (BF*)(ws + 25282560);
+    p.fc1T2  = (BF*)(ws + 25315328);
+    p.fc2T2  = (BF*)(ws + 25446400);
+
+    void* args[] = { &p };
+    hipLaunchCooperativeKernel((void*)mega_kernel, dim3(512), dim3(256),
+                               args, 0, stream);
 }
```
